# Kernel tuning notes

Hardware: AMD Instinct MI355X
Metric: run time of the kernel (lower is better)

The kernel has to match this reference:

```python
import jax, jax.numpy as jnp
import numpy as np

SUB1 = 0.5
SUB2 = 0.2


def setup_inputs() -> dict:
    key = jax.random.key(0)
    k1, k2, k3 = jax.random.split(key, 3)
    x = jax.random.normal(k1, (32, 64, 128, 128), dtype=jnp.float32)
    conv_weight = jax.random.normal(k2, (128, 64, 3, 3), dtype=jnp.float32) * 0.05
    conv_bias = jax.random.normal(k3, (128,), dtype=jnp.float32) * 0.05
    return {"x": x, "conv_weight": conv_weight, "conv_bias": conv_bias}


def reference(x, conv_weight, conv_bias):
    # Conv2d, stride 1, VALID padding (kernel computes out_h = in_h - K + 1)
    y = jax.lax.conv_general_dilated(
        x, conv_weight,
        window_strides=(1, 1), padding="VALID",
        dimension_numbers=("NCHW", "OIHW", "NCHW"))
    y = y + conv_bias[None, :, None, None]
    v = y - SUB1 - SUB2
    # Mish: v * tanh(softplus(v)); softplus == log(1 + exp(v)) (stable form)
    return v * jnp.tanh(jax.nn.softplus(v))
```

## Files before the change

### kernel.cpp

```cpp
#include <hip/hip_runtime.h>
#include <hip/hip_bf16.h>

typedef short bf16x8 __attribute__((ext_vector_type(8)));
typedef float f32x4 __attribute__((ext_vector_type(4)));

constexpr int C_IN = 64, H_IN = 128, W_IN = 128, C_OUT = 128, OH = 126, OW = 126;
constexpr int PAD = 72;
constexpr float SUBC = 0.7f;

constexpr size_t WR_BYTES = (size_t)9 * C_OUT * C_IN * 2;
constexpr size_t XB_BYTES = (size_t)32 * H_IN * W_IN * C_IN * 2;

__global__ void reorder_weights(const float* __restrict__ w, __hip_bfloat16* __restrict__ wr) {
    int o = blockIdx.x * 256 + threadIdx.x;
    if (o >= 9 * C_OUT * C_IN) return;
    int ci = o & 63;
    int co = (o >> 6) & 127;
    int k9 = o >> 13;
    int kh = k9 / 3, kw = k9 % 3;
    wr[o] = __float2bfloat16(w[((co * C_IN + ci) * 3 + kh) * 3 + kw]);
}

__global__ __launch_bounds__(256) void convert_x(const float* __restrict__ x, __hip_bfloat16* __restrict__ xb) {
    int b   = blockIdx.x;
    int tid = threadIdx.x;
    const float* src = x + (size_t)(b >> 7) * C_IN * H_IN * W_IN + (size_t)(b & 127) * W_IN;
    __hip_bfloat16* dst = xb + (size_t)b * (W_IN * C_IN);
    for (int r = 0; r < 4; ++r) {
        int t  = tid + r * 256;
        int cb = t & 7;
        int w  = t >> 3;
        alignas(16) __hip_bfloat16 tmp[8];
        #pragma unroll
        for (int e = 0; e < 8; ++e)
            tmp[e] = __float2bfloat16(src[(size_t)(cb * 8 + e) * (H_IN * W_IN) + w]);
        *(bf16x8*)&dst[w * C_IN + cb * 8] = *(const bf16x8*)tmp;
    }
}

template <bool PRE>
__global__ __launch_bounds__(256, 2) void conv_mish(
    const float* __restrict__ x, const __hip_bfloat16* __restrict__ xb,
    const __hip_bfloat16* __restrict__ wr,
    const float* __restrict__ bias, float* __restrict__ out)
{
    __shared__ __hip_bfloat16 Xs[128 * PAD];
    __shared__ __hip_bfloat16 Bs[128 * PAD];

    int b = blockIdx.x;
    int lb = (b & 7) * 504 + (b >> 3);
    int n  = lb / OH;
    int oh = lb % OH;

    int tid  = threadIdx.x;
    int lane = tid & 63;
    int wv   = tid >> 6;
    int wm   = wv >> 1;
    int wn   = wv & 1;
    int quad = lane >> 4;
    int l16  = lane & 15;

    f32x4 acc[4][4] = {};

    for (int kh = 0; kh < 3; ++kh) {
        __syncthreads();
        if (PRE) {
            const __hip_bfloat16* xrow = xb + ((size_t)n * H_IN + (oh + kh)) * (W_IN * C_IN);
            for (int r = 0; r < 4; ++r) {
                int t  = tid + r * 256;
                int cb = t & 7;
                int w  = t >> 3;
                *(bf16x8*)&Xs[w * PAD + cb * 8] = *(const bf16x8*)(xrow + w * C_IN + cb * 8);
            }
        } else {
            const float* xn = x + (size_t)n * C_IN * H_IN * W_IN;
            int h = oh + kh;
            for (int r = 0; r < 4; ++r) {
                int t  = tid + r * 256;
                int w  = t & 127;
                int cb = t >> 7;
                const float* gp = xn + ((size_t)(cb * 8) * H_IN + h) * W_IN + w;
                alignas(16) __hip_bfloat16 tmp[8];
                #pragma unroll
                for (int e = 0; e < 8; ++e)
                    tmp[e] = __float2bfloat16(gp[(size_t)e * (H_IN * W_IN)]);
                *(bf16x8*)&Xs[w * PAD + cb * 8] = *(const bf16x8*)tmp;
            }
        }
        {
            const __hip_bfloat16* src = wr + ((kh * 3 + 0) << 13);
            for (int r = 0; r < 4; ++r) {
                int c   = tid + r * 256;
                int co  = c >> 3;
                int ci8 = (c & 7) << 3;
                *(bf16x8*)&Bs[co * PAD + ci8] = *(const bf16x8*)(src + co * 64 + ci8);
            }
        }
        __syncthreads();

        for (int kw = 0; kw < 3; ++kw) {
            if (kw) {
                __syncthreads();
                const __hip_bfloat16* src = wr + ((kh * 3 + kw) << 13);
                for (int r = 0; r < 4; ++r) {
                    int c   = tid + r * 256;
                    int co  = c >> 3;
                    int ci8 = (c & 7) << 3;
                    *(bf16x8*)&Bs[co * PAD + ci8] = *(const bf16x8*)(src + co * 64 + ci8);
                }
                __syncthreads();
            }
            #pragma unroll
            for (int half = 0; half < 2; ++half) {
                int k0 = half * 32 + quad * 8;
                bf16x8 a[4], bf[4];
                #pragma unroll
                for (int j = 0; j < 4; ++j) {
                    int co = wn * 64 + j * 16 + l16;
                    bf[j] = *(const bf16x8*)&Bs[co * PAD + k0];
                }
                #pragma unroll
                for (int i = 0; i < 4; ++i) {
                    int m = wm * 64 + i * 16 + l16;
                    int widx = m + kw; if (widx > 127) widx = 127;
                    a[i] = *(const bf16x8*)&Xs[widx * PAD + k0];
                }
                #pragma unroll
                for (int i = 0; i < 4; ++i)
                    #pragma unroll
                    for (int j = 0; j < 4; ++j)
                        acc[i][j] = __builtin_amdgcn_mfma_f32_16x16x32_bf16(a[i], bf[j], acc[i][j], 0, 0, 0);
            }
        }
    }

    for (int j = 0; j < 4; ++j) {
        int co = wn * 64 + j * 16 + l16;
        float bb = bias[co] - SUBC;
        for (int i = 0; i < 4; ++i) {
            int ow0 = wm * 64 + i * 16 + quad * 4;
            float o[4];
            for (int r = 0; r < 4; ++r) {
                float v = acc[i][j][r] + bb;
                float e = __expf(v);
                float t = e * (e + 2.0f);
                float m = v * t * __builtin_amdgcn_rcpf(t + 2.0f);
                o[r] = (v > 20.0f) ? v : m;
            }
            float* dst = out + (((size_t)n * C_OUT + co) * OH + oh) * OW + ow0;
            float2 p0; p0.x = o[0]; p0.y = o[1];
            *(float2*)dst = p0;
            if (ow0 + 2 < OW) {
                float2 p1; p1.x = o[2]; p1.y = o[3];
                *(float2*)(dst + 2) = p1;
            }
        }
    }
}

extern "C" void kernel_launch(void* const* d_in, const int* in_sizes, int n_in,
                              void* d_out, int out_size, void* d_ws, size_t ws_size,
                              hipStream_t stream) {
    const float* x    = (const float*)d_in[0];
    const float* w    = (const float*)d_in[1];
    const float* bias = (const float*)d_in[2];
    float* out        = (float*)d_out;
    __hip_bfloat16* wr = (__hip_bfloat16*)d_ws;

    reorder_weights<<<(9 * C_OUT * C_IN + 255) / 256, 256, 0, stream>>>(w, wr);

    if (ws_size >= WR_BYTES + XB_BYTES) {
        __hip_bfloat16* xb = (__hip_bfloat16*)((char*)d_ws + WR_BYTES);
        convert_x<<<32 * H_IN, 256, 0, stream>>>(x, xb);
        conv_mish<true><<<32 * OH, 256, 0, stream>>>(x, xb, wr, bias, out);
    } else {
        conv_mish<false><<<32 * OH, 256, 0, stream>>>(x, nullptr, wr, bias, out);
    }
}
```

Baseline: 445.1 us.

## Double-buffer conv staging with direct global-to-LDS loads and XOR-swizzled layouts

Replaces the padded LDS tiles with an XOR-swizzled 64-channel layout, applied at preprocessing time to both weights and converted activations. The main conv kernel now stages input rows and per-tap weights straight into LDS with global_load_lds, double-buffered so the next tap's weights and next input row load while the current MFMAs run. This is meant to hide load latency, remove register round-trips, avoid LDS bank conflicts and halve the number of barriers. In exchange it uses 64KB of shared memory per block, which may limit occupancy.

New measurement: 450.5 us. No clear change (+1.2%).

```diff
diff --git a/kernel.cpp b/kernel.cpp
--- a/kernel.cpp
+++ b/kernel.cpp
@@ -10,6 +10,12 @@
 
 constexpr size_t WR_BYTES = (size_t)9 * C_OUT * C_IN * 2;
 constexpr size_t XB_BYTES = (size_t)32 * H_IN * W_IN * C_IN * 2;
+
+__device__ __forceinline__ void gl_lds16(const void* g, void* l) {
+    __builtin_amdgcn_global_load_lds(
+        (const __attribute__((address_space(1))) unsigned int*)g,
+        (__attribute__((address_space(3))) unsigned int*)l, 16, 0, 0);
+}
 
 __global__ void reorder_weights(const float* __restrict__ w, __hip_bfloat16* __restrict__ wr) {
     int o = blockIdx.x * 256 + threadIdx.x;
@@ -18,13 +24,15 @@
     int co = (o >> 6) & 127;
     int k9 = o >> 13;
     int kh = k9 / 3, kw = k9 % 3;
-    wr[o] = __float2bfloat16(w[((co * C_IN + ci) * 3 + kh) * 3 + kw]);
+    int cb = ci >> 3, e = ci & 7;
+    int dst = (k9 << 13) + (co << 6) + (((cb ^ co) & 7) << 3) + e;
+    wr[dst] = __float2bfloat16(w[((co * C_IN + ci) * 3 + kh) * 3 + kw]);
 }
 
 __global__ __launch_bounds__(256) void convert_x(const float* __restrict__ x, __hip_bfloat16* __restrict__ xb) {
     int b   = blockIdx.x;
     int tid = threadIdx.x;
-    const float* src = x + (size_t)(b >> 7) * C_IN * H_IN * W_IN + (size_t)(b & 127) * W_IN;
+    const float* src = x + (size_t)(b >> 7) * (C_IN * H_IN * W_IN) + (size_t)(b & 127) * W_IN;
     __hip_bfloat16* dst = xb + (size_t)b * (W_IN * C_IN);
     for (int r = 0; r < 4; ++r) {
         int t  = tid + r * 256;
@@ -34,20 +42,17 @@
         #pragma unroll
         for (int e = 0; e < 8; ++e)
             tmp[e] = __float2bfloat16(src[(size_t)(cb * 8 + e) * (H_IN * W_IN) + w]);
-        *(bf16x8*)&dst[w * C_IN + cb * 8] = *(const bf16x8*)tmp;
-    }
-}
-
-template <bool PRE>
-__global__ __launch_bounds__(256, 2) void conv_mish(
-    const float* __restrict__ x, const __hip_bfloat16* __restrict__ xb,
-    const __hip_bfloat16* __restrict__ wr,
+        *(bf16x8*)&dst[(w << 6) + (((cb ^ w) & 7) << 3)] = *(const bf16x8*)tmp;
+    }
+}
+
+__global__ __launch_bounds__(256, 2) void conv_mish_pipe(
+    const __hip_bfloat16* __restrict__ xb, const __hip_bfloat16* __restrict__ wr,
     const float* __restrict__ bias, float* __restrict__ out)
 {
-    __shared__ __hip_bfloat16 Xs[128 * PAD];
-    __shared__ __hip_bfloat16 Bs[128 * PAD];
-
-    int b = blockIdx.x;
+    __shared__ alignas(16) __hip_bfloat16 smem[4 * 8192];
+
+    int b  = blockIdx.x;
     int lb = (b & 7) * 504 + (b >> 3);
     int n  = lb / OH;
     int oh = lb % OH;
@@ -62,18 +67,102 @@
 
     f32x4 acc[4][4] = {};
 
+    const __hip_bfloat16* xbase = xb + ((size_t)n * H_IN + oh) * (W_IN * C_IN);
+
+    auto stage = [&](const __hip_bfloat16* src, __hip_bfloat16* dst) {
+        const char* s = (const char*)src + (wv << 12) + (lane << 4);
+        char* d = (char*)dst + (wv << 12);
+        #pragma unroll
+        for (int r = 0; r < 4; ++r)
+            gl_lds16(s + r * 1024, d + r * 1024);
+    };
+
+    stage(xbase, smem);
+    stage(wr, smem + 2 * 8192);
+    __syncthreads();
+
+    for (int s = 0; s < 9; ++s) {
+        int kh = s / 3, kw = s - kh * 3;
+        int p = s & 1, q = kh & 1;
+        if (s < 8) stage(wr + (size_t)(s + 1) * 8192, smem + (2 + (p ^ 1)) * 8192);
+        if (kw == 0 && kh < 2) stage(xbase + (size_t)(kh + 1) * (W_IN * C_IN), smem + (q ^ 1) * 8192);
+
+        const __hip_bfloat16* Xp = smem + q * 8192;
+        const __hip_bfloat16* Bp = smem + (2 + p) * 8192;
+        #pragma unroll
+        for (int half = 0; half < 2; ++half) {
+            int g = half * 4 + quad;
+            bf16x8 a[4], bfr[4];
+            #pragma unroll
+            for (int j = 0; j < 4; ++j) {
+                int co = wn * 64 + j * 16 + l16;
+                bfr[j] = *(const bf16x8*)&Bp[(co << 6) + (((g ^ co) & 7) << 3)];
+            }
+            #pragma unroll
+            for (int i = 0; i < 4; ++i) {
+                int m = wm * 64 + i * 16 + l16 + kw;
+                int widx = m > 127 ? 127 : m;
+                a[i] = *(const bf16x8*)&Xp[(widx << 6) + (((g ^ widx) & 7) << 3)];
+            }
+            #pragma unroll
+            for (int i = 0; i < 4; ++i)
+                #pragma unroll
+                for (int j = 0; j < 4; ++j)
+                    acc[i][j] = __builtin_amdgcn_mfma_f32_16x16x32_bf16(a[i], bfr[j], acc[i][j], 0, 0, 0);
+        }
+        if (s < 8) __syncthreads();
+    }
+
+    for (int j = 0; j < 4; ++j) {
+        int co = wn * 64 + j * 16 + l16;
+        float bb = bias[co] - SUBC;
+        for (int i = 0; i < 4; ++i) {
+            int ow0 = wm * 64 + i * 16 + quad * 4;
+            float o[4];
+            for (int r = 0; r < 4; ++r) {
+                float v = acc[i][j][r] + bb;
+                float e = __expf(v);
+                float t = e * (e + 2.0f);
+                float m = v * t * __builtin_amdgcn_rcpf(t + 2.0f);
+                o[r] = (v > 20.0f) ? v : m;
+            }
+            float* dst = out + (((size_t)n * C_OUT + co) * OH + oh) * OW + ow0;
+            float2 p0; p0.x = o[0]; p0.y = o[1];
+            *(float2*)dst = p0;
+            if (ow0 + 2 < OW) {
+                float2 p1; p1.x = o[2]; p1.y = o[3];
+                *(float2*)(dst + 2) = p1;
+            }
+        }
+    }
+}
+
+__global__ __launch_bounds__(256, 2) void conv_mish_legacy(
+    const float* __restrict__ x, const __hip_bfloat16* __restrict__ wr,
+    const float* __restrict__ bias, float* __restrict__ out)
+{
+    __shared__ __hip_bfloat16 Xs[128 * PAD];
+    __shared__ __hip_bfloat16 Bs[128 * PAD];
+
+    int b = blockIdx.x;
+    int lb = (b & 7) * 504 + (b >> 3);
+    int n  = lb / OH;
+    int oh = lb % OH;
+
+    int tid  = threadIdx.x;
+    int lane = tid & 63;
+    int wv   = tid >> 6;
+    int wm   = wv >> 1;
+    int wn   = wv & 1;
+    int quad = lane >> 4;
+    int l16  = lane & 15;
+
+    f32x4 acc[4][4] = {};
+    const float* xn = x + (size_t)n * C_IN * H_IN * W_IN;
+
     for (int kh = 0; kh < 3; ++kh) {
         __syncthreads();
-        if (PRE) {
-            const __hip_bfloat16* xrow = xb + ((size_t)n * H_IN + (oh + kh)) * (W_IN * C_IN);
-            for (int r = 0; r < 4; ++r) {
-                int t  = tid + r * 256;
-                int cb = t & 7;
-                int w  = t >> 3;
-                *(bf16x8*)&Xs[w * PAD + cb * 8] = *(const bf16x8*)(xrow + w * C_IN + cb * 8);
-            }
-        } else {
-            const float* xn = x + (size_t)n * C_IN * H_IN * W_IN;
+        {
             int h = oh + kh;
             for (int r = 0; r < 4; ++r) {
                 int t  = tid + r * 256;
@@ -113,11 +202,12 @@
             #pragma unroll
             for (int half = 0; half < 2; ++half) {
                 int k0 = half * 32 + quad * 8;
-                bf16x8 a[4], bf[4];
+                int g  = half * 4 + quad;
+                bf16x8 a[4], bfr[4];
                 #pragma unroll
                 for (int j = 0; j < 4; ++j) {
                     int co = wn * 64 + j * 16 + l16;
-                    bf[j] = *(const bf16x8*)&Bs[co * PAD + k0];
+                    bfr[j] = *(const bf16x8*)&Bs[co * PAD + (((g ^ co) & 7) << 3)];
                 }
                 #pragma unroll
                 for (int i = 0; i < 4; ++i) {
@@ -129,7 +219,7 @@
                 for (int i = 0; i < 4; ++i)
                     #pragma unroll
                     for (int j = 0; j < 4; ++j)
-                        acc[i][j] = __builtin_amdgcn_mfma_f32_16x16x32_bf16(a[i], bf[j], acc[i][j], 0, 0, 0);
+                        acc[i][j] = __builtin_amdgcn_mfma_f32_16x16x32_bf16(a[i], bfr[j], acc[i][j], 0, 0, 0);
             }
         }
     }
@@ -172,8 +262,8 @@
     if (ws_size >= WR_BYTES + XB_BYTES) {
         __hip_bfloat16* xb = (__hip_bfloat16*)((char*)d_ws + WR_BYTES);
         convert_x<<<32 * H_IN, 256, 0, stream>>>(x, xb);
-        conv_mish<true><<<32 * OH, 256, 0, stream>>>(x, xb, wr, bias, out);
+        conv_mish_pipe<<<32 * OH, 256, 0, stream>>>(xb, wr, bias, out);
     } else {
-        conv_mish<false><<<32 * OH, 256, 0, stream>>>(x, nullptr, wr, bias, out);
-    }
-}
+        conv_mish_legacy<<<32 * OH, 256, 0, stream>>>(x, wr, bias, out);
+    }
+}
```
